# Optimization experiments

Measured on AMD Instinct MI355X. Metric: run time of the kernel, lower is better.

## Reference

```python
import jax, jax.numpy as jnp
import numpy as np

N_POS = 1024
ALPHA = 0.3
B, S = 32, 1024


def setup_inputs() -> dict:
    key = jax.random.key(0)
    k1, k2, k3, k4 = jax.random.split(key, 4)
    s_arc = jax.random.normal(k1, (B, S, S), dtype=jnp.float32)
    a_arc = jax.random.normal(k2, (B, S, S), dtype=jnp.float32)
    adds = jax.random.randint(k3, (B, S), 0, N_POS, dtype=jnp.int32)
    pos = jax.random.randint(k4, (B, S), 0, N_POS, dtype=jnp.int32)
    return {"s_arc": s_arc, "a_arc": a_arc, "adds": adds, "pos": pos}


def reference(s_arc, a_arc, adds, pos):
    n_bins = N_POS * N_POS
    # --- histogram (scatter-add) of a_arc by POS-pair index ---
    # original: _add[b,p1,p2] = adds[b,p1]*seq_len + adds[b,p2]
    sl = adds.shape[1]
    pair_idx = adds[:, :, None] * sl + adds[:, None, :]            # [B,S,S]
    # indices >= n_bins never match any bin in the original masked-sum loop;
    # segment_sum with num_segments=n_bins drops them identically.
    hist = jax.ops.segment_sum(a_arc.reshape(-1), pair_idx.reshape(-1),
                               num_segments=n_bins)                # [n_pos^2]
    score_arc = jax.nn.sigmoid(hist)
    # --- gather score back into s_arc ---
    slp = pos.shape[1]
    pidx = pos[:, :, None] * slp + pos[:, None, :]                  # [B,S,S]
    valid = pidx < n_bins
    gathered = score_arc[jnp.clip(pidx, 0, n_bins - 1)]
    return s_arc + ALPHA * jnp.where(valid, gathered, jnp.float32(0))
```

## Files before the change

### kernel.cpp

```cpp
#include <hip/hip_runtime.h>

#define NPOS 1024
#define BB   32
#define SS   1024
#define ALPHA_C 0.3f
#define OCAP 256
#define MAXO 16
#define PADPAIR 0x10001000u
#define SSTRIDE 1026
#define NZ4 16656
#define NP4 16384

typedef float    __attribute__((ext_vector_type(2))) f32x2;
typedef float    __attribute__((ext_vector_type(4))) f32x4;
typedef int      __attribute__((ext_vector_type(4))) i32x4;
typedef unsigned __attribute__((ext_vector_type(4))) u32x4;

__global__ __launch_bounds__(256) void fill_tables(u32x4* __restrict__ z,
                                                   u32x4* __restrict__ p) {
    const int i = blockIdx.x * 256 + threadIdx.x;
    if (i < NZ4) z[i] = (u32x4){0u, 0u, 0u, 0u};
    else { const int j = i - NZ4; if (j < NP4) p[j] = (u32x4){PADPAIR, PADPAIR, PADPAIR, PADPAIR}; }
}

__global__ __launch_bounds__(256) void build_tables(
    const int* __restrict__ adds, unsigned* __restrict__ rcnt,
    unsigned* __restrict__ scnt, unsigned* __restrict__ bmask,
    ushort* __restrict__ list, ushort* __restrict__ ell16,
    int* __restrict__ ocntc, int* __restrict__ ocntr,
    int* __restrict__ oentc, int* __restrict__ oentr) {
    const int b  = blockIdx.x >> 2;
    const int tg = ((blockIdx.x & 3) << 8) | threadIdx.x;
    const int c  = adds[b * SS + tg];
    const unsigned slot = atomicAdd(&scnt[b * NPOS + c], 1u);
    if (slot < 4u) {
        ell16[(((size_t)b * 512 + (c & 511)) * 2 + (c >> 9)) * 4 + slot] = (ushort)(tg << 2);
    } else {
        const int o = atomicAdd(&ocntc[b], 1);
        if (o < OCAP) oentc[b * OCAP + o] = (c << 10) | tg;
    }
    const unsigned rs = atomicAdd(&rcnt[c * BB + b], 1u);
    if (rs < 4u) {
        list[(size_t)c * 128 + b * 4 + rs] = (ushort)tg;
    } else {
        const int o = atomicAdd(&ocntr[b], 1);
        if (o < OCAP) oentr[b * OCAP + o] = (c << 10) | tg;
        atomicOr(&bmask[b * 32 + (tg >> 5)], 1u << (tg & 31));
    }
}

__global__ __launch_bounds__(512) void hist_rows_kernel(
    const float* __restrict__ a, const unsigned* __restrict__ rcnt,
    const ushort* __restrict__ list, const ushort* __restrict__ ell16,
    float* __restrict__ hist) {
    __shared__ float Sbuf[2][SSTRIDE];
    __shared__ ushort lsrc[128];
    __shared__ int   mcnt_s[32];
    __shared__ ushort actb_s[32];
    __shared__ int   na_s;
    const int r = blockIdx.x, t = threadIdx.x;

    if (t < 128) lsrc[t] = list[(size_t)r * 128 + t];
    if (t < 32)  mcnt_s[t] = min((int)rcnt[r * BB + t], 4);
    if (t < 2)   Sbuf[t][1024] = 0.f;
    __syncthreads();
    if (t == 0) {
        int na = 0;
        for (int b = 0; b < 32; ++b) if (mcnt_s[b]) actb_s[na++] = (ushort)b;
        na_s = na;
    }
    __syncthreads();
    const int na = na_s;
    const u32x4* ellv = (const u32x4*)ell16;
    float acc0 = 0.f, acc1 = 0.f;
    u32x4 E = (u32x4){PADPAIR, PADPAIR, PADPAIR, PADPAIR}, F = E;
    f32x2 R0 = (f32x2){0.f, 0.f}, R1 = R0, R2 = R0, R3 = R0;
    f32x2 T0 = R0, T1 = R0, T2 = R0, T3 = R0;
    int mR = 0, mT = 0;

#define ROWP(bb, s) ((const f32x2*)(a + ((((size_t)(bb) << 10) + lsrc[(bb) * 4 + (s)]) << 10)) + t)

    if (na > 0) {
        const int b0 = actb_s[0], m0 = mcnt_s[b0];
        E = ellv[(size_t)b0 * 512 + t];
        f32x2 S = __builtin_nontemporal_load(ROWP(b0, 0));
        if (m0 > 1) S += __builtin_nontemporal_load(ROWP(b0, 1));
        if (m0 > 2) S += __builtin_nontemporal_load(ROWP(b0, 2));
        if (m0 > 3) S += __builtin_nontemporal_load(ROWP(b0, 3));
        ((f32x2*)&Sbuf[0][0])[t] = S;
        if (na > 1) {
            const int b1 = actb_s[1];
            mR = mcnt_s[b1];
            F = ellv[(size_t)b1 * 512 + t];
            R0 = __builtin_nontemporal_load(ROWP(b1, 0));
            if (mR > 1) R1 = __builtin_nontemporal_load(ROWP(b1, 1));
            if (mR > 2) R2 = __builtin_nontemporal_load(ROWP(b1, 2));
            if (mR > 3) R3 = __builtin_nontemporal_load(ROWP(b1, 3));
        }
        if (na > 2) {
            const int b2 = actb_s[2];
            mT = mcnt_s[b2];
            T0 = __builtin_nontemporal_load(ROWP(b2, 0));
            if (mT > 1) T1 = __builtin_nontemporal_load(ROWP(b2, 1));
            if (mT > 2) T2 = __builtin_nontemporal_load(ROWP(b2, 2));
            if (mT > 3) T3 = __builtin_nontemporal_load(ROWP(b2, 3));
        }
    }
    asm volatile("s_waitcnt lgkmcnt(0)" ::: "memory");
    __builtin_amdgcn_s_barrier();

    for (int j = 0; j < na; ++j) {
        f32x2 U0 = (f32x2){0.f, 0.f}, U1 = U0, U2 = U0, U3 = U0;
        int mU = 0;
        if (j + 3 < na) {
            const int b3 = actb_s[j + 3];
            mU = mcnt_s[b3];
            U0 = __builtin_nontemporal_load(ROWP(b3, 0));
            if (mU > 1) U1 = __builtin_nontemporal_load(ROWP(b3, 1));
            if (mU > 2) U2 = __builtin_nontemporal_load(ROWP(b3, 2));
            if (mU > 3) U3 = __builtin_nontemporal_load(ROWP(b3, 3));
        }
        u32x4 TE = (u32x4){PADPAIR, PADPAIR, PADPAIR, PADPAIR};
        if (j + 2 < na) TE = ellv[(size_t)actb_s[j + 2] * 512 + t];
        if (j + 1 < na) {
            f32x2 S = R0;
            if (mR > 1) S += R1;
            if (mR > 2) S += R2;
            if (mR > 3) S += R3;
            ((f32x2*)&Sbuf[(j + 1) & 1][0])[t] = S;
        }
        const char* rb = (const char*)&Sbuf[j & 1][0];
        acc0 += *(const float*)(rb + (E.x & 0xffffu));
        acc0 += *(const float*)(rb + (E.x >> 16));
        acc0 += *(const float*)(rb + (E.y & 0xffffu));
        acc0 += *(const float*)(rb + (E.y >> 16));
        acc1 += *(const float*)(rb + (E.z & 0xffffu));
        acc1 += *(const float*)(rb + (E.z >> 16));
        acc1 += *(const float*)(rb + (E.w & 0xffffu));
        acc1 += *(const float*)(rb + (E.w >> 16));
        E = F; F = TE;
        R0 = T0; R1 = T1; R2 = T2; R3 = T3; mR = mT;
        T0 = U0; T1 = U1; T2 = U2; T3 = U3; mT = mU;
        __builtin_amdgcn_sched_barrier(0);
        asm volatile("s_waitcnt lgkmcnt(0)" ::: "memory");
        __builtin_amdgcn_s_barrier();
    }
#undef ROWP

    const size_t o0 = (size_t)r * NPOS + t;
    hist[o0]       = acc0;
    hist[o0 + 512] = acc1;
}

__global__ __launch_bounds__(256) void fixup(
    const float* __restrict__ a, const int* __restrict__ adds,
    const int* __restrict__ ocntc, const int* __restrict__ oentc,
    const int* __restrict__ ocntr, const int* __restrict__ oentr,
    const unsigned* __restrict__ bmask, float* __restrict__ hist) {
    const int b = blockIdx.x;
    int y = blockIdx.y;
    const int p = blockIdx.z * 256 + threadIdx.x;
    if (y < MAXO) {
        if (y >= ocntc[b]) return;
        const int e = oentc[b * OCAP + y];
        const int c = e >> 10, p2 = e & 1023;
        if ((bmask[b * 32 + (p >> 5)] >> (p & 31)) & 1u) return;
        const int r = adds[b * SS + p];
        atomicAdd(&hist[(size_t)r * NPOS + c], a[((size_t)(b * SS + p)) * SS + p2]);
    } else {
        y -= MAXO;
        if (y >= ocntr[b]) return;
        const int e = oentr[b * OCAP + y];
        const int r = e >> 10, p1 = e & 1023;
        const int c = adds[b * SS + p];
        atomicAdd(&hist[(size_t)r * NPOS + c], a[((size_t)(b * SS + p1)) * SS + p]);
    }
}

__global__ __launch_bounds__(256) void gather_kernel(
    const float* __restrict__ s, const int* __restrict__ pos,
    const float* __restrict__ score, float* __restrict__ out) {
    __shared__ float srow[NPOS];
    const int row = blockIdx.x;
    const int b   = row >> 10;
    const int*  posb = pos + b * SS;
    const int   base = posb[row & 1023] * NPOS;
    const size_t off = (size_t)row * SS;
    const int t = threadIdx.x;

    const f32x4 sc = ((const f32x4*)(score + base))[t];
    f32x4 v = __builtin_nontemporal_load(((const f32x4*)(s + off)) + t);
    i32x4 c = ((const i32x4*)posb)[t];
    ((f32x4*)srow)[t] = sc;
    __syncthreads();

    const float h0 = srow[c.x], h1 = srow[c.y];
    const float h2 = srow[c.z], h3 = srow[c.w];
    f32x4 o;
    o.x = v.x + ALPHA_C * (1.f / (1.f + __expf(-h0)));
    o.y = v.y + ALPHA_C * (1.f / (1.f + __expf(-h1)));
    o.z = v.z + ALPHA_C * (1.f / (1.f + __expf(-h2)));
    o.w = v.w + ALPHA_C * (1.f / (1.f + __expf(-h3)));
    __builtin_nontemporal_store(o, ((f32x4*)(out + off)) + t);
}

extern "C" void kernel_launch(void* const* d_in, const int* in_sizes, int n_in,
                              void* d_out, int out_size, void* d_ws, size_t ws_size,
                              hipStream_t stream) {
    const float* s_arc = (const float*)d_in[0];
    const float* a_arc = (const float*)d_in[1];
    const int*   adds  = (const int*)d_in[2];
    const int*   pos   = (const int*)d_in[3];
    float* out  = (float*)d_out;

    char* w = (char*)d_ws;
    float*    hist  = (float*)w;                 w += (size_t)NPOS * NPOS * 4;
    unsigned* rcnt  = (unsigned*)w;              w += (size_t)NPOS * BB * 4;
    unsigned* scnt  = (unsigned*)w;              w += (size_t)BB * NPOS * 4;
    unsigned* bmask = (unsigned*)w;              w += (size_t)BB * 32 * 4;
    int*      ocntc = (int*)w;                   w += BB * 4;
    int*      ocntr = (int*)w;                   w += BB * 4;
    ushort*   list  = (ushort*)w;                w += (size_t)NPOS * 128 * 2;
    ushort*   ell16 = (ushort*)w;                w += (size_t)BB * NPOS * 4 * 2;
    int*      oentc = (int*)w;                   w += (size_t)BB * OCAP * 4;
    int*      oentr = (int*)w;

    fill_tables<<<(NZ4 + NP4 + 255) / 256, 256, 0, stream>>>((u32x4*)rcnt, (u32x4*)ell16);
    build_tables<<<4 * BB, 256, 0, stream>>>(adds, rcnt, scnt, bmask, list, ell16,
                                             ocntc, ocntr, oentc, oentr);
    hist_rows_kernel<<<NPOS, 512, 0, stream>>>(a_arc, rcnt, list, ell16, hist);
    fixup<<<dim3(BB, 2 * MAXO, SS / 256), 256, 0, stream>>>(a_arc, adds, ocntc, oentc,
                                                            ocntr, oentr, bmask, hist);
    gather_kernel<<<BB * SS, 256, 0, stream>>>(s_arc, pos, hist, out);
}
```

Before: 116.3 us.

## Split histogram row accumulation across two blocks with separate partial buffers

Each histogram row is now processed by two blocks, each handling alternating active batches and writing to its own partial histogram buffer. The gather kernel sums the two partial rows before applying the sigmoid. This doubles the grid size to expose more parallelism and memory-level concurrency in the streaming row loads. In exchange it adds an extra histogram buffer, an extra score-row read per gather block, and shorter software pipelines per block.

New measurement: 139.6 us. 1.2x slower.

```diff
diff --git a/kernel.cpp b/kernel.cpp
--- a/kernel.cpp
+++ b/kernel.cpp
@@ -52,13 +52,13 @@
 __global__ __launch_bounds__(512) void hist_rows_kernel(
     const float* __restrict__ a, const unsigned* __restrict__ rcnt,
     const ushort* __restrict__ list, const ushort* __restrict__ ell16,
-    float* __restrict__ hist) {
+    float* __restrict__ hist0, float* __restrict__ hist1) {
     __shared__ float Sbuf[2][SSTRIDE];
     __shared__ ushort lsrc[128];
     __shared__ int   mcnt_s[32];
     __shared__ ushort actb_s[32];
     __shared__ int   na_s;
-    const int r = blockIdx.x, t = threadIdx.x;
+    const int r = blockIdx.x >> 1, h = blockIdx.x & 1, t = threadIdx.x;
 
     if (t < 128) lsrc[t] = list[(size_t)r * 128 + t];
     if (t < 32)  mcnt_s[t] = min((int)rcnt[r * BB + t], 4);
@@ -70,7 +70,9 @@
         na_s = na;
     }
     __syncthreads();
-    const int na = na_s;
+    const int na  = na_s;
+    const int nah = (na > h) ? ((na - h + 1) >> 1) : 0;
+#define AB(i) ((int)actb_s[(((i) << 1) | h)])
     const u32x4* ellv = (const u32x4*)ell16;
     float acc0 = 0.f, acc1 = 0.f;
     u32x4 E = (u32x4){PADPAIR, PADPAIR, PADPAIR, PADPAIR}, F = E;
@@ -80,16 +82,16 @@
 
 #define ROWP(bb, s) ((const f32x2*)(a + ((((size_t)(bb) << 10) + lsrc[(bb) * 4 + (s)]) << 10)) + t)
 
-    if (na > 0) {
-        const int b0 = actb_s[0], m0 = mcnt_s[b0];
+    if (nah > 0) {
+        const int b0 = AB(0), m0 = mcnt_s[b0];
         E = ellv[(size_t)b0 * 512 + t];
         f32x2 S = __builtin_nontemporal_load(ROWP(b0, 0));
         if (m0 > 1) S += __builtin_nontemporal_load(ROWP(b0, 1));
         if (m0 > 2) S += __builtin_nontemporal_load(ROWP(b0, 2));
         if (m0 > 3) S += __builtin_nontemporal_load(ROWP(b0, 3));
         ((f32x2*)&Sbuf[0][0])[t] = S;
-        if (na > 1) {
-            const int b1 = actb_s[1];
+        if (nah > 1) {
+            const int b1 = AB(1);
             mR = mcnt_s[b1];
             F = ellv[(size_t)b1 * 512 + t];
             R0 = __builtin_nontemporal_load(ROWP(b1, 0));
@@ -97,8 +99,8 @@
             if (mR > 2) R2 = __builtin_nontemporal_load(ROWP(b1, 2));
             if (mR > 3) R3 = __builtin_nontemporal_load(ROWP(b1, 3));
         }
-        if (na > 2) {
-            const int b2 = actb_s[2];
+        if (nah > 2) {
+            const int b2 = AB(2);
             mT = mcnt_s[b2];
             T0 = __builtin_nontemporal_load(ROWP(b2, 0));
             if (mT > 1) T1 = __builtin_nontemporal_load(ROWP(b2, 1));
@@ -109,11 +111,11 @@
     asm volatile("s_waitcnt lgkmcnt(0)" ::: "memory");
     __builtin_amdgcn_s_barrier();
 
-    for (int j = 0; j < na; ++j) {
+    for (int i = 0; i < nah; ++i) {
         f32x2 U0 = (f32x2){0.f, 0.f}, U1 = U0, U2 = U0, U3 = U0;
         int mU = 0;
-        if (j + 3 < na) {
-            const int b3 = actb_s[j + 3];
+        if (i + 3 < nah) {
+            const int b3 = AB(i + 3);
             mU = mcnt_s[b3];
             U0 = __builtin_nontemporal_load(ROWP(b3, 0));
             if (mU > 1) U1 = __builtin_nontemporal_load(ROWP(b3, 1));
@@ -121,15 +123,15 @@
             if (mU > 3) U3 = __builtin_nontemporal_load(ROWP(b3, 3));
         }
         u32x4 TE = (u32x4){PADPAIR, PADPAIR, PADPAIR, PADPAIR};
-        if (j + 2 < na) TE = ellv[(size_t)actb_s[j + 2] * 512 + t];
-        if (j + 1 < na) {
+        if (i + 2 < nah) TE = ellv[(size_t)AB(i + 2) * 512 + t];
+        if (i + 1 < nah) {
             f32x2 S = R0;
             if (mR > 1) S += R1;
             if (mR > 2) S += R2;
             if (mR > 3) S += R3;
-            ((f32x2*)&Sbuf[(j + 1) & 1][0])[t] = S;
-        }
-        const char* rb = (const char*)&Sbuf[j & 1][0];
+            ((f32x2*)&Sbuf[(i + 1) & 1][0])[t] = S;
+        }
+        const char* rb = (const char*)&Sbuf[i & 1][0];
         acc0 += *(const float*)(rb + (E.x & 0xffffu));
         acc0 += *(const float*)(rb + (E.x >> 16));
         acc0 += *(const float*)(rb + (E.y & 0xffffu));
@@ -146,10 +148,12 @@
         __builtin_amdgcn_s_barrier();
     }
 #undef ROWP
-
+#undef AB
+
+    float* histh = h ? hist1 : hist0;
     const size_t o0 = (size_t)r * NPOS + t;
-    hist[o0]       = acc0;
-    hist[o0 + 512] = acc1;
+    histh[o0]       = acc0;
+    histh[o0 + 512] = acc1;
 }
 
 __global__ __launch_bounds__(256) void fixup(
@@ -179,7 +183,8 @@
 
 __global__ __launch_bounds__(256) void gather_kernel(
     const float* __restrict__ s, const int* __restrict__ pos,
-    const float* __restrict__ score, float* __restrict__ out) {
+    const float* __restrict__ score0, const float* __restrict__ score1,
+    float* __restrict__ out) {
     __shared__ float srow[NPOS];
     const int row = blockIdx.x;
     const int b   = row >> 10;
@@ -188,10 +193,11 @@
     const size_t off = (size_t)row * SS;
     const int t = threadIdx.x;
 
-    const f32x4 sc = ((const f32x4*)(score + base))[t];
+    const f32x4 sc0 = ((const f32x4*)(score0 + base))[t];
+    const f32x4 sc1 = ((const f32x4*)(score1 + base))[t];
     f32x4 v = __builtin_nontemporal_load(((const f32x4*)(s + off)) + t);
     i32x4 c = ((const i32x4*)posb)[t];
-    ((f32x4*)srow)[t] = sc;
+    ((f32x4*)srow)[t] = sc0 + sc1;
     __syncthreads();
 
     const float h0 = srow[c.x], h1 = srow[c.y];
@@ -214,7 +220,8 @@
     float* out  = (float*)d_out;
 
     char* w = (char*)d_ws;
-    float*    hist  = (float*)w;                 w += (size_t)NPOS * NPOS * 4;
+    float*    hist0 = (float*)w;                 w += (size_t)NPOS * NPOS * 4;
+    float*    hist1 = (float*)w;                 w += (size_t)NPOS * NPOS * 4;
     unsigned* rcnt  = (unsigned*)w;              w += (size_t)NPOS * BB * 4;
     unsigned* scnt  = (unsigned*)w;              w += (size_t)BB * NPOS * 4;
     unsigned* bmask = (unsigned*)w;              w += (size_t)BB * 32 * 4;
@@ -228,8 +235,8 @@
     fill_tables<<<(NZ4 + NP4 + 255) / 256, 256, 0, stream>>>((u32x4*)rcnt, (u32x4*)ell16);
     build_tables<<<4 * BB, 256, 0, stream>>>(adds, rcnt, scnt, bmask, list, ell16,
                                              ocntc, ocntr, oentc, oentr);
-    hist_rows_kernel<<<NPOS, 512, 0, stream>>>(a_arc, rcnt, list, ell16, hist);
+    hist_rows_kernel<<<2 * NPOS, 512, 0, stream>>>(a_arc, rcnt, list, ell16, hist0, hist1);
     fixup<<<dim3(BB, 2 * MAXO, SS / 256), 256, 0, stream>>>(a_arc, adds, ocntc, oentc,
-                                                            ocntr, oentr, bmask, hist);
-    gather_kernel<<<BB * SS, 256, 0, stream>>>(s_arc, pos, hist, out);
-}
+                                                            ocntr, oentr, bmask, hist0);
+    gather_kernel<<<BB * SS, 256, 0, stream>>>(s_arc, pos, hist0, hist1, out);
+}
```
